# Kernel optimization log

Hardware: AMD Instinct MI355X
Metric: run time of the kernel (lower is better)

## Reference

```python
import jax, jax.numpy as jnp
import numpy as np

NHLOG2PI = -0.5 * np.log(2.0 * np.pi)


def _log_bessel_i(nu, x):
    # log I_nu(x) via the uniform asymptotic expansion (A&S 9.7.7), accurate for large nu.
    # Replaces the original mpmath besseli loop with a device-friendly closed form.
    z = x / nu
    sq = jnp.sqrt(1.0 + z * z)
    eta = sq + jnp.log(z) - jnp.log1p(sq)
    t = 1.0 / sq
    u1 = (3.0 * t - 5.0 * t ** 3) / 24.0  # first correction term
    return nu * eta - 0.5 * jnp.log(2.0 * jnp.pi * nu) - 0.25 * jnp.log1p(z * z) + jnp.log1p(u1 / nu)


def _log_vmf_partition(d, kappa):
    # log C_d(kappa) = d*(-0.5 log 2pi) + s*log(kappa) - log I_s(kappa), s = d/2 - 1
    s = 0.5 * d - 1.0
    return d * NHLOG2PI + s * jnp.log(kappa) - _log_bessel_i(s, kappa)


def reference(id_samples, kappa_weight, prototypes, targets, project_dim):
    eps_n = 1e-12  # torch F.normalize eps
    eps_c = 1e-8   # torch cosine_similarity eps
    # --- sequential normalized EMA scatter-update of prototypes (faithful to per-sample loop) ---
    norm_samples = id_samples / jnp.maximum(
        jnp.linalg.norm(id_samples, axis=-1, keepdims=True), eps_n)

    def step(protos, inp):
        s_n, t = inp
        new = 0.05 * s_n + 0.95 * protos[t]
        new = new / jnp.maximum(jnp.linalg.norm(new), eps_n)
        return protos.at[t].set(new), None

    protos, _ = jax.lax.scan(step, prototypes, (norm_samples, targets))
    protos = jax.lax.stop_gradient(protos)  # original uses .data.detach()

    # --- cosine similarity [N, C] without materializing the repeated tensors ---
    x_n = id_samples / jnp.maximum(jnp.linalg.norm(id_samples, axis=-1, keepdims=True), eps_c)
    p_n = protos / jnp.maximum(jnp.linalg.norm(protos, axis=-1, keepdims=True), eps_c)
    cos = x_n @ p_n.T  # [N, C]

    kap = jax.nn.relu(kappa_weight)  # [C]
    logits = cos * kap[None, :]
    weight_before_exp = jnp.exp(_log_vmf_partition(float(project_dim), kap))[None, :]  # [1, C]

    # --- weighted vMF NLL ---
    num = weight_before_exp * jnp.exp(logits)
    pred = num / num.sum(-1, keepdims=True)
    p_t = jnp.take_along_axis(pred, targets[:, None], axis=1)[:, 0]
    return -jnp.mean(jnp.log(p_t + 1e-6))


def setup_inputs() -> dict:
    key = jax.random.key(0)
    k1, k2, k3 = jax.random.split(key, 3)
    N, C, D = 16384, 2048, 32
    return {
        "id_samples": jax.random.normal(k1, (N, D), dtype=jnp.float32),
        "kappa_weight": jax.random.uniform(k2, (C,), dtype=jnp.float32),
        "prototypes": jnp.zeros((C, D), dtype=jnp.float32),
        "targets": jax.random.randint(k3, (N,), 0, C),
        "project_dim": D,
    }
```

## Files before the change

### kernel.cpp

```cpp
#include <hip/hip_runtime.h>
#include <hip/hip_bf16.h>
#include <math.h>

#define D 32
#define CAP 28
#define CPB 4
#define SBT 512
#define SSM 16

typedef __attribute__((ext_vector_type(8))) short short8v;
typedef __attribute__((ext_vector_type(4))) float float4v;

static __device__ __forceinline__ unsigned short f2bf(float f) {
    union { __hip_bfloat16 h; unsigned short u; } cv;
    cv.h = __float2bfloat16(f);
    return cv.u;
}
static __device__ __forceinline__ short8v cvt8(float4 u0, float4 u1) {
    short8v o;
    o[0] = (short)f2bf(u0.x); o[1] = (short)f2bf(u0.y);
    o[2] = (short)f2bf(u0.z); o[3] = (short)f2bf(u0.w);
    o[4] = (short)f2bf(u1.x); o[5] = (short)f2bf(u1.y);
    o[6] = (short)f2bf(u1.z); o[7] = (short)f2bf(u1.w);
    return o;
}

__global__ void __launch_bounds__(64 * CPB)
k_gram(const float* __restrict__ x, const int* __restrict__ tgt,
       const float* __restrict__ p_in, const float* __restrict__ kw,
       unsigned short* __restrict__ qb, float* __restrict__ w,
       int N, int C, float dval) {
    __shared__ int   lcnt[CPB];
    __shared__ int   llist[CPB][CAP];
    __shared__ int   slist[CPB][CAP];
    __shared__ float Graw[CPB][32][33];
    __shared__ float invv[CPB][32];
    __shared__ float gamS[CPB][CAP];
    int tid = threadIdx.x, b = blockIdx.x;
    int lane = tid & 63, wv = tid >> 6;
    int c = b * CPB + wv, e = lane & 31;

    if (tid < CPB) lcnt[tid] = 0;
    __syncthreads();
    for (int i = tid; i < N; i += 64 * CPB) {
        int r = tgt[i] - b * CPB;
        if ((unsigned)r < (unsigned)CPB) {
            int pos = atomicAdd(&lcnt[r], 1);
            if (pos < CAP) llist[r][pos] = i;
        }
    }
    __syncthreads();

    int n = lcnt[wv];
    float kap = fmaxf(kw[c], 0.0f);

    if (n <= CAP) {
        int idx = (lane < n) ? llist[wv][lane] : 0x7fffffff;
        int rank = 0;
        for (int j = 0; j < n; ++j) { int v = __shfl(idx, j); rank += (v < idx) ? 1 : 0; }
        if (lane < n) slist[wv][rank] = idx;

        int m = lane & 15, kg = lane >> 4, k0 = kg * 8;
        short8v A0 = {0,0,0,0,0,0,0,0}, A1 = {0,0,0,0,0,0,0,0};
        if (m < n) {
            const float4* px = (const float4*)(x + (size_t)slist[wv][m] * D + k0);
            A0 = cvt8(px[0], px[1]);
        }
        {
            int r = 16 + m;
            if (r < n) {
                const float4* px = (const float4*)(x + (size_t)slist[wv][r] * D + k0);
                A1 = cvt8(px[0], px[1]);
            } else if (r == 31) {
                const float4* px = (const float4*)(p_in + (size_t)c * D + k0);
                A1 = cvt8(px[0], px[1]);
            }
        }
        float4v z = {0.f, 0.f, 0.f, 0.f};
        float4v g00 = __builtin_amdgcn_mfma_f32_16x16x32_bf16(A0, A0, z, 0, 0, 0);
        float4v g01 = __builtin_amdgcn_mfma_f32_16x16x32_bf16(A0, A1, z, 0, 0, 0);
        float4v g10 = __builtin_amdgcn_mfma_f32_16x16x32_bf16(A1, A0, z, 0, 0, 0);
        float4v g11 = __builtin_amdgcn_mfma_f32_16x16x32_bf16(A1, A1, z, 0, 0, 0);
#pragma unroll
        for (int r = 0; r < 4; ++r) {
            int rr = kg * 4 + r;
            Graw[wv][rr][m]           = g00[r];
            Graw[wv][rr][16 + m]      = g01[r];
            Graw[wv][16 + rr][m]      = g10[r];
            Graw[wv][16 + rr][16 + m] = g11[r];
        }
        if (lane < 32)
            invv[wv][lane] = 1.0f / fmaxf(sqrtf(Graw[wv][lane][lane]), 1e-12f);

        float B = 1.0f, U2 = Graw[wv][31][31];
        for (int kk = 0; kk < n; ++kk) {
            const float* grow = &Graw[wv][kk][0];
            float a0 = 0.f, a1 = 0.f, a2 = 0.f, a3 = 0.f;
            int j = 0;
            for (; j + 4 <= kk; j += 4) {
                a0 = fmaf(gamS[wv][j],     grow[j],     a0);
                a1 = fmaf(gamS[wv][j + 1], grow[j + 1], a1);
                a2 = fmaf(gamS[wv][j + 2], grow[j + 2], a2);
                a3 = fmaf(gamS[wv][j + 3], grow[j + 3], a3);
            }
            for (; j < kk; ++j) a0 = fmaf(gamS[wv][j], grow[j], a0);
            float dot = grow[31] + ((a0 + a1) + (a2 + a3));
            float dsum = invv[wv][kk] * B * dot;
            float m2 = 0.0025f + fmaf(0.9025f, U2, 0.095f * dsum);
            float mm = fmaxf(sqrtf(m2), 1e-12f);
            B *= 0.95f / mm;
            float gk = (0.05f * invv[wv][kk]) / (mm * B);
            if (lane == 0) gamS[wv][kk] = gk;
            U2 = 1.0f;
        }

        float u = p_in[(size_t)c * D + e];
        for (int j = 0; j < n; ++j)
            u = fmaf(gamS[wv][j], x[(size_t)slist[wv][j] * D + e], u);
        float ss = u * u;
        ss += __shfl_xor(ss, 16); ss += __shfl_xor(ss, 8); ss += __shfl_xor(ss, 4);
        ss += __shfl_xor(ss, 2);  ss += __shfl_xor(ss, 1);
        float pninv = 1.0f / fmaxf(sqrtf(ss), 1e-8f);
        if (lane < D) qb[(size_t)c * D + e] = f2bf(kap * pninv * u);
    } else {
        float p = p_in[(size_t)c * D + e];
        for (int ii = 0; ii < N; ii += 64) {
            unsigned long long mb = __ballot(tgt[ii + lane] == c);
            while (mb) {
                int j = __ffsll(mb) - 1;
                mb &= (mb - 1);
                float v = x[(size_t)(ii + j) * D + e];
                float s2 = v * v;
                s2 += __shfl_xor(s2, 16); s2 += __shfl_xor(s2, 8); s2 += __shfl_xor(s2, 4);
                s2 += __shfl_xor(s2, 2);  s2 += __shfl_xor(s2, 1);
                float s = v / fmaxf(sqrtf(s2), 1e-12f);
                p = fmaf(0.05f, s, 0.95f * p);
                float pp = p * p;
                pp += __shfl_xor(pp, 16); pp += __shfl_xor(pp, 8); pp += __shfl_xor(pp, 4);
                pp += __shfl_xor(pp, 2);  pp += __shfl_xor(pp, 1);
                p = p / fmaxf(sqrtf(pp), 1e-12f);
            }
        }
        float pp = p * p;
        pp += __shfl_xor(pp, 16); pp += __shfl_xor(pp, 8); pp += __shfl_xor(pp, 4);
        pp += __shfl_xor(pp, 2);  pp += __shfl_xor(pp, 1);
        float pn = p / fmaxf(sqrtf(pp), 1e-8f);
        if (lane < D) qb[(size_t)c * D + e] = f2bf(kap * pn);
    }

    if (lane == 0) {
        float nu = 0.5f * dval - 1.0f;
        float zz = kap / nu, z2 = zz * zz;
        float sq = sqrtf(1.0f + z2);
        float t  = 1.0f / sq;
        float u1 = (3.0f * t - 5.0f * t * t * t) * (1.0f / 24.0f);
        float lw = dval * (-0.918938533204672742f)
                 + nu * (logf(nu) + log1pf(sq) - sq)
                 + 0.5f * logf(6.2831853071795864f * nu)
                 + 0.25f * log1pf(z2)
                 - log1pf(u1 / nu);
        w[c] = __expf(lw);
    }
}

__global__ void __launch_bounds__(SBT)
k_score(const float* __restrict__ x, const int* __restrict__ tgt,
        const unsigned short* __restrict__ qb, const float* __restrict__ w,
        float* __restrict__ part, int N, int C) {
    __shared__ float Sl[8][SSM];
    __shared__ float Lt[SSM];
    int tid = threadIdx.x, b = blockIdx.x;
    int lane = tid & 63, wv = tid >> 6;
    int m = lane & 15, kg = lane >> 4, k0 = kg * 8;
    int s0 = b * SSM;

    short8v a0;
    {
        const float4* px = (const float4*)(x + (size_t)(s0 + m) * D + k0);
        float4 u0 = px[0], u1 = px[1];
        float ss = u0.x*u0.x + u0.y*u0.y + u0.z*u0.z + u0.w*u0.w
                 + u1.x*u1.x + u1.y*u1.y + u1.z*u1.z + u1.w*u1.w;
        ss += __shfl_xor(ss, 16); ss += __shfl_xor(ss, 32);
        float inv = 1.0f / fmaxf(sqrtf(ss), 1e-8f);
        float4 v0, v1;
        v0.x = u0.x*inv; v0.y = u0.y*inv; v0.z = u0.z*inv; v0.w = u0.w*inv;
        v1.x = u1.x*inv; v1.y = u1.y*inv; v1.z = u1.z*inv; v1.w = u1.w*inv;
        a0 = cvt8(v0, v1);
    }

    int tr0[4];
#pragma unroll
    for (int r = 0; r < 4; ++r) tr0[r] = tgt[s0 + kg * 4 + r];

    float4v z = {0.f, 0.f, 0.f, 0.f};
    float4v sa0 = z;
    int ntiles = C >> 7;
    for (int jt = 0; jt < ntiles; ++jt) {
        int c0 = (wv * ntiles + jt) * 16;
        short8v bfrag = *(const short8v*)(qb + (size_t)(c0 + m) * D + k0);
        float wl = w[c0 + m];
        float4v acc0 = __builtin_amdgcn_mfma_f32_16x16x32_bf16(a0, bfrag, z, 0, 0, 0);
#pragma unroll
        for (int r = 0; r < 4; ++r) {
            if (c0 + m == tr0[r]) Lt[kg * 4 + r] = acc0[r];
            sa0[r] = fmaf(wl, __expf(acc0[r]), sa0[r]);
        }
    }
#pragma unroll
    for (int off = 1; off < 16; off <<= 1) {
#pragma unroll
        for (int r = 0; r < 4; ++r) sa0[r] += __shfl_xor(sa0[r], off);
    }
    if (m == 0) {
#pragma unroll
        for (int r = 0; r < 4; ++r) Sl[wv][kg * 4 + r] = sa0[r];
    }
    __syncthreads();

    if (wv == 0) {
        float val = 0.f;
        if (lane < SSM) {
            int s = lane;
            float S = ((Sl[0][s] + Sl[1][s]) + (Sl[2][s] + Sl[3][s]))
                    + ((Sl[4][s] + Sl[5][s]) + (Sl[6][s] + Sl[7][s]));
            int t = tgt[s0 + s];
            val = logf(w[t] * __expf(Lt[s]) / S + 1e-6f);
        }
        val += __shfl_xor(val, 32); val += __shfl_xor(val, 16); val += __shfl_xor(val, 8);
        val += __shfl_xor(val, 4);  val += __shfl_xor(val, 2);  val += __shfl_xor(val, 1);
        if (lane == 0) part[b] = val;
    }
}

__global__ void k_out(const float* __restrict__ part, float* __restrict__ out,
                      int N, int nblk) {
    __shared__ float red[8];
    int tid = threadIdx.x, lane = tid & 63, wv = tid >> 6;
    float v = 0.f;
    if (tid < nblk)       v += part[tid];
    if (tid + 512 < nblk) v += part[tid + 512];
    v += __shfl_xor(v, 32); v += __shfl_xor(v, 16); v += __shfl_xor(v, 8);
    v += __shfl_xor(v, 4);  v += __shfl_xor(v, 2);  v += __shfl_xor(v, 1);
    if (lane == 0) red[wv] = v;
    __syncthreads();
    if (tid == 0)
        out[0] = -(((red[0] + red[1]) + (red[2] + red[3]))
                 + ((red[4] + red[5]) + (red[6] + red[7]))) / (float)N;
}

extern "C" void kernel_launch(void* const* d_in, const int* in_sizes, int n_in,
                              void* d_out, int out_size, void* d_ws, size_t ws_size,
                              hipStream_t stream) {
    const float* x    = (const float*)d_in[0];
    const float* kw   = (const float*)d_in[1];
    const float* p_in = (const float*)d_in[2];
    const int*   tgt  = (const int*)d_in[3];
    int C = in_sizes[1];
    int N = in_sizes[3];
    float dval = (float)(in_sizes[2] / C);
    int nblk = N / SSM;

    unsigned short* qb = (unsigned short*)d_ws;
    float* w    = (float*)(qb + (size_t)C * D);
    float* part = w + C;
    (void)n_in; (void)out_size; (void)ws_size;

    k_gram<<<C / CPB, 64 * CPB, 0, stream>>>(x, tgt, p_in, kw, qb, w, N, C, dval);
    k_score<<<nblk, SBT, 0, stream>>>(x, tgt, qb, w, part, N, C);
    k_out<<<1, 512, 0, stream>>>(part, (float*)d_out, N, nblk);
}
```

Before: 41.21 us.

## Bucket targets in a global pre-pass and reuse MFMA operands for prototype sum

Before, every k_gram block scanned all N targets to find the samples of its own classes. That scan is replaced by a separate bucketing kernel that uses global atomics to build per-class index lists, preceded by a memset. The final prototype accumulation also changes: instead of re-reading fp32 x rows, it reuses the bf16 operands already held in registers and combines them with shuffle reductions. This removes redundant global reads, but it adds two extra launches and uses bf16-rounded inputs for the final prototype vector.

```diff
diff --git a/kernel.cpp b/kernel.cpp
--- a/kernel.cpp
+++ b/kernel.cpp
@@ -15,6 +15,11 @@
     union { __hip_bfloat16 h; unsigned short u; } cv;
     cv.h = __float2bfloat16(f);
     return cv.u;
+}
+static __device__ __forceinline__ float bf2f(unsigned short u) {
+    union { float f; unsigned int i; } c;
+    c.i = ((unsigned int)u) << 16;
+    return c.f;
 }
 static __device__ __forceinline__ short8v cvt8(float4 u0, float4 u1) {
     short8v o;
@@ -25,13 +30,22 @@
     return o;
 }
 
+__global__ void k_bucket(const int* __restrict__ tgt, int* __restrict__ cnt,
+                         int* __restrict__ list2d, int N) {
+    int i = blockIdx.x * blockDim.x + threadIdx.x;
+    if (i < N) {
+        int t = tgt[i];
+        int pos = atomicAdd(&cnt[t], 1);
+        if (pos < CAP) list2d[t * CAP + pos] = i;
+    }
+}
+
 __global__ void __launch_bounds__(64 * CPB)
 k_gram(const float* __restrict__ x, const int* __restrict__ tgt,
+       const int* __restrict__ cnt, const int* __restrict__ list2d,
        const float* __restrict__ p_in, const float* __restrict__ kw,
        unsigned short* __restrict__ qb, float* __restrict__ w,
        int N, int C, float dval) {
-    __shared__ int   lcnt[CPB];
-    __shared__ int   llist[CPB][CAP];
     __shared__ int   slist[CPB][CAP];
     __shared__ float Graw[CPB][32][33];
     __shared__ float invv[CPB][32];
@@ -40,22 +54,11 @@
     int lane = tid & 63, wv = tid >> 6;
     int c = b * CPB + wv, e = lane & 31;
 
-    if (tid < CPB) lcnt[tid] = 0;
-    __syncthreads();
-    for (int i = tid; i < N; i += 64 * CPB) {
-        int r = tgt[i] - b * CPB;
-        if ((unsigned)r < (unsigned)CPB) {
-            int pos = atomicAdd(&lcnt[r], 1);
-            if (pos < CAP) llist[r][pos] = i;
-        }
-    }
-    __syncthreads();
-
-    int n = lcnt[wv];
+    int n = cnt[c];
     float kap = fmaxf(kw[c], 0.0f);
 
     if (n <= CAP) {
-        int idx = (lane < n) ? llist[wv][lane] : 0x7fffffff;
+        int idx = (lane < n) ? list2d[c * CAP + lane] : 0x7fffffff;
         int rank = 0;
         for (int j = 0; j < n; ++j) { int v = __shfl(idx, j); rank += (v < idx) ? 1 : 0; }
         if (lane < n) slist[wv][rank] = idx;
@@ -114,14 +117,32 @@
             U2 = 1.0f;
         }
 
-        float u = p_in[(size_t)c * D + e];
-        for (int j = 0; j < n; ++j)
-            u = fmaf(gamS[wv][j], x[(size_t)slist[wv][j] * D + e], u);
-        float ss = u * u;
-        ss += __shfl_xor(ss, 16); ss += __shfl_xor(ss, 8); ss += __shfl_xor(ss, 4);
-        ss += __shfl_xor(ss, 2);  ss += __shfl_xor(ss, 1);
-        float pninv = 1.0f / fmaxf(sqrtf(ss), 1e-8f);
-        if (lane < D) qb[(size_t)c * D + e] = f2bf(kap * pninv * u);
+        float coef0 = (m < n) ? gamS[wv][m] : 0.0f;
+        float coef1 = (16 + m < n) ? gamS[wv][16 + m] : ((16 + m == 31) ? 1.0f : 0.0f);
+        float part[8];
+#pragma unroll
+        for (int jj = 0; jj < 8; ++jj)
+            part[jj] = fmaf(coef0, bf2f((unsigned short)A0[jj]),
+                            coef1 * bf2f((unsigned short)A1[jj]));
+#pragma unroll
+        for (int off = 1; off < 16; off <<= 1) {
+#pragma unroll
+            for (int jj = 0; jj < 8; ++jj)
+                part[jj] += __shfl_xor(part[jj], off);
+        }
+        float ssl = 0.f;
+#pragma unroll
+        for (int jj = 0; jj < 8; ++jj) ssl = fmaf(part[jj], part[jj], ssl);
+        ssl += __shfl_xor(ssl, 16);
+        ssl += __shfl_xor(ssl, 32);
+        float pninv = 1.0f / fmaxf(sqrtf(ssl), 1e-8f);
+        float sc = kap * pninv;
+        if (m == 0) {
+            short8v ov;
+#pragma unroll
+            for (int jj = 0; jj < 8; ++jj) ov[jj] = (short)f2bf(sc * part[jj]);
+            *(short8v*)(qb + (size_t)c * D + k0) = ov;
+        }
     } else {
         float p = p_in[(size_t)c * D + e];
         for (int ii = 0; ii < N; ii += 64) {
@@ -260,12 +281,16 @@
     float dval = (float)(in_sizes[2] / C);
     int nblk = N / SSM;
 
-    unsigned short* qb = (unsigned short*)d_ws;
+    int* cnt    = (int*)d_ws;
+    int* list2d = cnt + C;
+    unsigned short* qb = (unsigned short*)(list2d + (size_t)C * CAP);
     float* w    = (float*)(qb + (size_t)C * D);
     float* part = w + C;
     (void)n_in; (void)out_size; (void)ws_size;
 
-    k_gram<<<C / CPB, 64 * CPB, 0, stream>>>(x, tgt, p_in, kw, qb, w, N, C, dval);
+    hipMemsetAsync(cnt, 0, (size_t)C * sizeof(int), stream);
+    k_bucket<<<(N + 255) / 256, 256, 0, stream>>>(tgt, cnt, list2d, N);
+    k_gram<<<C / CPB, 64 * CPB, 0, stream>>>(x, tgt, cnt, list2d, p_in, kw, qb, w, N, C, dval);
     k_score<<<nblk, SBT, 0, stream>>>(x, tgt, qb, w, part, N, C);
     k_out<<<1, 512, 0, stream>>>(part, (float*)d_out, N, nblk);
 }
```

Measured after the change: 40.75 us. No clear change (-1.1%).
